# Kernel tuning notes

Hardware: AMD Instinct MI355X
Metric: run time of the kernel (lower is better)

Reference implementation:

```python
import jax, jax.numpy as jnp
import numpy as np

HEADS = 4
BN_EPS = 1e-5


def _linear_attention(x, heads):
    # x: [B, L, C]; per-head linear attention: softmax(Q,dim=feat) @ (softmax(K,dim=seq)^T @ V)
    B, L, C = x.shape
    dh = C // heads
    h = x.reshape(B, L, heads, dh)
    q = jax.nn.softmax(h, axis=-1)          # softmax over feature dim (dim=2 in torch)
    k = jax.nn.softmax(h, axis=1)           # softmax over sequence dim (dim=1 in torch)
    kv = jnp.einsum('blhd,blhe->bhde', k, h)   # [B, H, dh, dh]
    out = jnp.einsum('blhd,bhde->blhe', q, kv) # [B, L, H, dh]
    return out.reshape(B, L, C)


def setup_inputs() -> dict:
    key = jax.random.key(0)
    ks = jax.random.split(key, 10)
    B, C, L, DOUT, NB = 32, 32, 16384, 10, 3
    s = 0.1
    return {
        'x': jax.random.normal(ks[0], (B, C, L), jnp.float32),
        'fcW1': jax.random.normal(ks[1], (NB, C, C), jnp.float32) * s,
        'fcb1': jax.random.normal(ks[2], (NB, C), jnp.float32) * s,
        'fcW2': jax.random.normal(ks[3], (NB, C, C), jnp.float32) * s,
        'fcb2': jax.random.normal(ks[4], (NB, C), jnp.float32) * s,
        'Wh': jax.random.normal(ks[5], (C, C), jnp.float32) * s,
        'bh': jax.random.normal(ks[6], (C,), jnp.float32) * s,
        'bn_gamma': jnp.ones((C,), jnp.float32),
        'bn_beta': jnp.zeros((C,), jnp.float32),
        'bn_mean': jnp.zeros((C,), jnp.float32),
        'bn_var': jnp.ones((C,), jnp.float32),
        'Wf': jax.random.normal(ks[7], (C, DOUT), jnp.float32) * s,
        'bf': jax.random.normal(ks[8], (DOUT,), jnp.float32) * s,
    }


def reference(x, fcW1, fcb1, fcW2, fcb2, Wh, bh, bn_gamma, bn_beta, bn_mean, bn_var, Wf, bf):
    gelu = lambda t: jax.nn.gelu(t, approximate=False)  # torch default GELU is exact erf
    h = jnp.transpose(x, (0, 2, 1))  # [B, C, L] -> [B, L, C]
    n_blocks = fcW1.shape[0]
    for i in range(n_blocks):
        h = _linear_attention(h, HEADS)
        h = gelu(h @ fcW1[i] + fcb1[i])
        h = gelu(h @ fcW2[i] + fcb2[i])
    pooled = jnp.mean(h, axis=1)  # AdaptiveAvgPool1d(1) over L -> [B, C]
    y = pooled @ Wh + bh
    y = (y - bn_mean) * jax.lax.rsqrt(bn_var + BN_EPS) * bn_gamma + bn_beta  # BatchNorm1d (eval)
    y = gelu(y)
    return y @ Wf + bf
```

## Files before the change

### kernel.cpp

```cpp
#include <hip/hip_runtime.h>
#include <cstddef>

#define B_ 32
#define C_ 32
#define L_ 16384
#define H_ 4
#define DH_ 8
#define NB_ 3
#define DOUT_ 10
#define SEG_ 512
#define S_ (L_/SEG_)

#define WTILE 512
#define AST  40

typedef _Float16 f16_t;
typedef _Float16 f16x2 __attribute__((ext_vector_type(2)));
typedef _Float16 f16x8 __attribute__((ext_vector_type(8)));
typedef float    f32x4 __attribute__((ext_vector_type(4)));

__device__ __forceinline__ float gelu_f(float x){
    const float z  = fabsf(x) * 0.70710678118654752440f;
    const float t  = __builtin_amdgcn_rcpf(fmaf(0.3275911f, z, 1.0f));
    const float e  = __expf(-z * z);
    float p = fmaf(t, 1.061405429f, -1.453152027f);
    p = fmaf(t, p, 1.421413741f);
    p = fmaf(t, p, -0.284496736f);
    p = fmaf(t, p, 0.254829592f);
    const float erfz = 1.0f - p * t * e;
    const float phi  = fmaf(copysignf(erfz, x), 0.5f, 0.5f);
    return x * phi;
}

#define RED_MAX32(v) do{ v = fmaxf(v, __shfl_xor(v,1));  v = fmaxf(v, __shfl_xor(v,2)); \
                         v = fmaxf(v, __shfl_xor(v,4));  v = fmaxf(v, __shfl_xor(v,8)); \
                         v = fmaxf(v, __shfl_xor(v,16)); }while(0)
#define RED_SUM32(v) do{ v += __shfl_xor(v,1);  v += __shfl_xor(v,2); \
                         v += __shfl_xor(v,4);  v += __shfl_xor(v,8); \
                         v += __shfl_xor(v,16); }while(0)

__global__ __launch_bounds__(256) void stats_kernel(const float* __restrict__ h,
                                                    float* __restrict__ part){
    const int seg = blockIdx.x;
    const int hd  = blockIdx.y;
    const int b   = blockIdx.z;
    const int t   = threadIdx.x;
    const int d   = t >> 5;
    const int j   = t & 31;

    __shared__ float tile[8][SEG_];
    __shared__ float sm[8];

    const float* hb = h + (size_t)b * ((size_t)C_*L_) + (size_t)(hd*DH_)*L_ + (size_t)seg*SEG_;

    for (int f = t; f < 8*SEG_/4; f += 256){
        const int row = f >> 7;
        const int c4  = (f & 127) << 2;
        *(f32x4*)&tile[row][c4] = *(const f32x4*)&hb[(size_t)row*L_ + c4];
    }
    __syncthreads();

    float m = -INFINITY;
    #pragma unroll
    for (int i = 0; i < SEG_/32; i++) m = fmaxf(m, tile[d][j + 32*i]);
    RED_MAX32(m);
    if (j == 0) sm[d] = m;
    const float m_d = m;

    float s = 0.0f;
    float kv[8];
    #pragma unroll
    for (int e = 0; e < 8; e++) kv[e] = 0.0f;
    #pragma unroll
    for (int i = 0; i < SEG_/32; i++){
        const int k = j + 32*i;
        const float ek = __expf(tile[d][k] - m_d);
        s += ek;
        #pragma unroll
        for (int e = 0; e < 8; e++) kv[e] = fmaf(ek, tile[e][k], kv[e]);
    }
    RED_SUM32(s);
    #pragma unroll
    for (int e = 0; e < 8; e++){ RED_SUM32(kv[e]); }
    __syncthreads();

    float* po = part + (size_t)((b*H_ + hd)*S_ + seg) * 80;
    if (j == 0){
        po[8 + d] = s;
        #pragma unroll
        for (int e = 0; e < 8; e++) po[16 + d*8 + e] = kv[e];
    }
    if (t < 8) po[t] = sm[t];
}

template<bool LAST>
__global__ __launch_bounds__(256)
__attribute__((amdgpu_waves_per_eu(3, 4)))
void block_kernel(const float* hin,
                  float* hout,
                  const float* __restrict__ part,
                  const float* __restrict__ W1,
                  const float* __restrict__ b1,
                  const float* __restrict__ W2,
                  const float* __restrict__ b2,
                  float* pooled,
                  unsigned* done_ctr,
                  const float* __restrict__ Wh,
                  const float* __restrict__ bh,
                  const float* __restrict__ gam,
                  const float* __restrict__ bet,
                  const float* __restrict__ mean,
                  const float* __restrict__ var,
                  const float* __restrict__ Wf,
                  const float* __restrict__ bf,
                  float* __restrict__ out){
    __shared__ __align__(16) f16_t Ash[256*AST];
    __shared__ f16_t Bsh1[32*AST];
    __shared__ f16_t Bsh2[32*AST];
    __shared__ float sb1[32], sb2[32];
    __shared__ float kvsh[256];
    __shared__ float pool[32];
    __shared__ unsigned lastf;

    const int tid = threadIdx.x;
    const int b   = blockIdx.y;
    const int l0  = blockIdx.x * WTILE;
    const size_t base = (size_t)b * ((size_t)C_*L_);

    float h0[32], h1[32];
    #pragma unroll
    for (int c = 0; c < 32; c++) h0[c] = hin[base + (size_t)c*L_ + l0 + tid];
    #pragma unroll
    for (int c = 0; c < 32; c++) h1[c] = hin[base + (size_t)c*L_ + l0 + 256 + tid];

    for (int i = tid; i < 1024; i += 256){
        const int k = i >> 5, n = i & 31;
        Bsh1[n*AST + k] = (f16_t)W1[i];
        Bsh2[n*AST + k] = (f16_t)W2[i];
    }
    if (tid < 32){ sb1[tid] = b1[tid]; sb2[tid] = b2[tid]; }
    if (LAST && tid < 32) pool[tid] = 0.0f;

    {
        const int hh_t = tid >> 6;
        const int tt   = tid & 63;
        const int dd   = tt >> 3;
        const float* pp = part + (size_t)(b*H_ + hh_t) * S_ * 80;
        float M = -INFINITY;
        for (int s2 = 0; s2 < S_; s2++) M = fmaxf(M, pp[s2*80 + dd]);
        float ssum = 0.0f, kvs = 0.0f;
        for (int s2 = 0; s2 < S_; s2++){
            const float sc = __expf(pp[s2*80 + dd] - M);
            ssum = fmaf(pp[s2*80 + 8  + dd], sc, ssum);
            kvs  = fmaf(pp[s2*80 + 16 + tt], sc, kvs);
        }
        kvsh[tid] = kvs / ssum;
    }
    __syncthreads();

    const int wv   = tid >> 6;
    const int lane = tid & 63;
    const int lr   = lane & 15;
    const int lk   = lane >> 4;
    const f32x4 zero = {0.f, 0.f, 0.f, 0.f};

    auto attn_to_ash = [&](const float (&hh)[32], const bool preb){
        float attn[32];
        #pragma unroll
        for (int hd2 = 0; hd2 < 4; hd2++){
            float mq = hh[hd2*8];
            #pragma unroll
            for (int d2 = 1; d2 < 8; d2++) mq = fmaxf(mq, hh[hd2*8 + d2]);
            float es[8]; float qs = 0.f;
            #pragma unroll
            for (int d2 = 0; d2 < 8; d2++){ es[d2] = __expf(hh[hd2*8 + d2] - mq); qs += es[d2]; }
            const float inv = __builtin_amdgcn_rcpf(qs);
            #pragma unroll
            for (int e = 0; e < 8; e++){
                float acc = 0.f;
                #pragma unroll
                for (int d2 = 0; d2 < 8; d2++) acc += es[d2] * kvsh[hd2*64 + d2*8 + e];
                attn[hd2*8 + e] = acc * inv;
            }
        }
        if (preb) __syncthreads();
        #pragma unroll
        for (int k2 = 0; k2 < 32; k2 += 2){
            f16x2 pr = { (f16_t)attn[k2], (f16_t)attn[k2+1] };
            *(f16x2*)&Ash[tid*AST + k2] = pr;
        }
    };

    auto fc_and_out = [&](const int lofs){
        f16x8 a[4], bw[2];
        f32x4 d[8];
        #pragma unroll
        for (int mt = 0; mt < 4; mt++)
            a[mt] = *(const f16x8*)&Ash[(wv*64 + mt*16 + lr)*AST + lk*8];
        #pragma unroll
        for (int nt = 0; nt < 2; nt++)
            bw[nt] = *(const f16x8*)&Bsh1[(nt*16 + lr)*AST + lk*8];
        #pragma unroll
        for (int nt = 0; nt < 2; nt++)
            #pragma unroll
            for (int mt = 0; mt < 4; mt++)
                d[nt*4+mt] = __builtin_amdgcn_mfma_f32_16x16x32_f16(a[mt], bw[nt], zero, 0, 0, 0);

        #pragma unroll
        for (int nt = 0; nt < 2; nt++){
            const float bias = sb1[nt*16 + lr];
            #pragma unroll
            for (int mt = 0; mt < 4; mt++)
                #pragma unroll
                for (int r = 0; r < 4; r++){
                    const float v = gelu_f(d[nt*4+mt][r] + bias);
                    Ash[(wv*64 + mt*16 + lk*4 + r)*AST + (nt*16 + lr)] = (f16_t)v;
                }
        }

        #pragma unroll
        for (int mt = 0; mt < 4; mt++)
            a[mt] = *(const f16x8*)&Ash[(wv*64 + mt*16 + lr)*AST + lk*8];
        #pragma unroll
        for (int nt = 0; nt < 2; nt++)
            bw[nt] = *(const f16x8*)&Bsh2[(nt*16 + lr)*AST + lk*8];
        #pragma unroll
        for (int nt = 0; nt < 2; nt++)
            #pragma unroll
            for (int mt = 0; mt < 4; mt++)
                d[nt*4+mt] = __builtin_amdgcn_mfma_f32_16x16x32_f16(a[mt], bw[nt], zero, 0, 0, 0);

        #pragma unroll
        for (int nt = 0; nt < 2; nt++){
            const float bias = sb2[nt*16 + lr];
            #pragma unroll
            for (int mt = 0; mt < 4; mt++)
                #pragma unroll
                for (int r = 0; r < 4; r++)
                    d[nt*4+mt][r] = gelu_f(d[nt*4+mt][r] + bias);
        }

        if (!LAST){
            #pragma unroll
            for (int nt = 0; nt < 2; nt++)
                #pragma unroll
                for (int mt = 0; mt < 4; mt++)
                    *(f32x4*)&hout[base + (size_t)(nt*16 + lr)*L_
                                   + l0 + lofs + wv*64 + mt*16 + lk*4] = d[nt*4+mt];
        } else {
            #pragma unroll
            for (int nt = 0; nt < 2; nt++){
                float ps = 0.f;
                #pragma unroll
                for (int mt = 0; mt < 4; mt++)
                    ps += d[nt*4+mt][0] + d[nt*4+mt][1] + d[nt*4+mt][2] + d[nt*4+mt][3];
                atomicAdd(&pool[nt*16 + lr], ps);
            }
        }
    };

    attn_to_ash(h0, false);
    __syncthreads();
    fc_and_out(0);
    attn_to_ash(h1, true);
    __syncthreads();
    fc_and_out(256);

    if (LAST){
        __syncthreads();
        if (tid < 32){
            atomicAdd(&pooled[b*32 + tid], pool[tid]);
            __threadfence();
        }
        __syncthreads();
        if (tid == 0){
            const unsigned old = atomicAdd(done_ctr, 1u);
            lastf = (old == 1023u) ? 1u : 0u;
        }
        __syncthreads();
        if (lastf){
            __threadfence();
            float* y2 = (float*)Ash;
            const float invL = 1.0f / (float)L_;
            for (int i = tid; i < 1024; i += 256){
                const int bb = i >> 5, cc = i & 31;
                float acc = bh[cc];
                #pragma unroll
                for (int dd2 = 0; dd2 < 32; dd2++)
                    acc += (pooled[bb*32 + dd2] * invL) * Wh[dd2*32 + cc];
                acc = (acc - mean[cc]) * rsqrtf(var[cc] + 1e-5f) * gam[cc] + bet[cc];
                y2[i] = gelu_f(acc);
            }
            __syncthreads();
            for (int i = tid; i < B_*DOUT_; i += 256){
                const int b2 = i / DOUT_, j = i % DOUT_;
                float r = bf[j];
                #pragma unroll
                for (int c2 = 0; c2 < 32; c2++) r += y2[b2*32 + c2] * Wf[c2*DOUT_ + j];
                out[i] = r;
            }
        }
    }
}

extern "C" void kernel_launch(void* const* d_in, const int* in_sizes, int n_in,
                              void* d_out, int out_size, void* d_ws, size_t ws_size,
                              hipStream_t stream){
    (void)in_sizes; (void)n_in; (void)out_size; (void)ws_size;
    const float* x    = (const float*)d_in[0];
    const float* fW1  = (const float*)d_in[1];
    const float* fb1  = (const float*)d_in[2];
    const float* fW2  = (const float*)d_in[3];
    const float* fb2  = (const float*)d_in[4];
    const float* Wh   = (const float*)d_in[5];
    const float* bh   = (const float*)d_in[6];
    const float* gam  = (const float*)d_in[7];
    const float* bet  = (const float*)d_in[8];
    const float* mean = (const float*)d_in[9];
    const float* var  = (const float*)d_in[10];
    const float* Wf   = (const float*)d_in[11];
    const float* bf   = (const float*)d_in[12];
    float* out = (float*)d_out;

    float* hbuf    = (float*)d_ws;
    float* part    = hbuf + (size_t)B_*C_*L_;
    float* pooled  = part + (size_t)B_*H_*S_*80;
    unsigned* done = (unsigned*)(pooled + B_*C_);

    hipMemsetAsync(pooled, 0, (B_*C_ + 1)*sizeof(float), stream);

    dim3 sgrid(S_, H_, B_);
    dim3 bgrid(L_/WTILE, B_);

    stats_kernel<<<sgrid, 256, 0, stream>>>(x, part);
    block_kernel<false><<<bgrid, 256, 0, stream>>>(x, hbuf, part,
        fW1, fb1, fW2, fb2, nullptr, nullptr,
        nullptr, nullptr, nullptr, nullptr, nullptr, nullptr, nullptr, nullptr, nullptr);
    stats_kernel<<<sgrid, 256, 0, stream>>>(hbuf, part);
    block_kernel<false><<<bgrid, 256, 0, stream>>>(hbuf, hbuf, part,
        fW1 + C_*C_, fb1 + C_, fW2 + C_*C_, fb2 + C_, nullptr, nullptr,
        nullptr, nullptr, nullptr, nullptr, nullptr, nullptr, nullptr, nullptr, nullptr);
    stats_kernel<<<sgrid, 256, 0, stream>>>(hbuf, part);
    block_kernel<true><<<bgrid, 256, 0, stream>>>(hbuf, nullptr, part,
        fW1 + 2*C_*C_, fb1 + 2*C_, fW2 + 2*C_*C_, fb2 + 2*C_, pooled, done,
        Wh, bh, gam, bet, mean, var, Wf, bf, out);
}
```

Before: 303.1 us.

## Fuse all stats and block phases into one persistent cooperative kernel

Replaces six separate kernel launches and the memset with a single cooperative persistent kernel that loops over layers. Stats and MLP work items are distributed across a fixed grid sized from occupancy, with grid.sync between phases. The final head runs on workgroup 0 after the last grid barrier instead of through an atomic done-counter. This removes launch gaps and tail effects, at the cost of grid-wide barriers and fewer blocks in flight per phase.

```diff
diff --git a/kernel.cpp b/kernel.cpp
--- a/kernel.cpp
+++ b/kernel.cpp
@@ -1,18 +1,29 @@
 #include <hip/hip_runtime.h>
+#include <hip/hip_cooperative_groups.h>
 #include <cstddef>
+
+namespace cg = cooperative_groups;
 
 #define B_ 32
 #define C_ 32
 #define L_ 16384
 #define H_ 4
-#define DH_ 8
 #define NB_ 3
 #define DOUT_ 10
 #define SEG_ 512
 #define S_ (L_/SEG_)
-
-#define WTILE 512
-#define AST  40
+#define NSU (B_*H_*S_)
+#define NPAIR (B_*(L_/256)/2)
+#define AST 40
+
+#define OFF_SM    16384
+#define OFF_B1    20480
+#define OFF_B2    23040
+#define OFF_SB1   25600
+#define OFF_SB2   25728
+#define OFF_KV    25856
+#define OFF_POOL  26880
+#define LDS_BYTES 27008
 
 typedef _Float16 f16_t;
 typedef _Float16 f16x2 __attribute__((ext_vector_type(2)));
@@ -39,266 +50,255 @@
                          v += __shfl_xor(v,4);  v += __shfl_xor(v,8); \
                          v += __shfl_xor(v,16); }while(0)
 
-__global__ __launch_bounds__(256) void stats_kernel(const float* __restrict__ h,
-                                                    float* __restrict__ part){
-    const int seg = blockIdx.x;
-    const int hd  = blockIdx.y;
-    const int b   = blockIdx.z;
-    const int t   = threadIdx.x;
-    const int d   = t >> 5;
-    const int j   = t & 31;
-
-    __shared__ float tile[8][SEG_];
-    __shared__ float sm[8];
-
-    const float* hb = h + (size_t)b * ((size_t)C_*L_) + (size_t)(hd*DH_)*L_ + (size_t)seg*SEG_;
-
-    for (int f = t; f < 8*SEG_/4; f += 256){
-        const int row = f >> 7;
-        const int c4  = (f & 127) << 2;
-        *(f32x4*)&tile[row][c4] = *(const f32x4*)&hb[(size_t)row*L_ + c4];
-    }
-    __syncthreads();
-
-    float m = -INFINITY;
-    #pragma unroll
-    for (int i = 0; i < SEG_/32; i++) m = fmaxf(m, tile[d][j + 32*i]);
-    RED_MAX32(m);
-    if (j == 0) sm[d] = m;
-    const float m_d = m;
-
-    float s = 0.0f;
-    float kv[8];
-    #pragma unroll
-    for (int e = 0; e < 8; e++) kv[e] = 0.0f;
-    #pragma unroll
-    for (int i = 0; i < SEG_/32; i++){
-        const int k = j + 32*i;
-        const float ek = __expf(tile[d][k] - m_d);
-        s += ek;
+template<bool LASTL>
+__device__ __forceinline__
+void block_phase(char* LB, const float* __restrict__ src, float* __restrict__ hbuf,
+                 const float* __restrict__ part,
+                 const float* __restrict__ W1, const float* __restrict__ b1w,
+                 const float* __restrict__ W2, const float* __restrict__ b2w,
+                 float* __restrict__ pooled,
+                 const int tid, const int wg, const int nwg)
+{
+    f16_t* Ash   = (f16_t*)LB;
+    f16_t* Bs1   = (f16_t*)(LB + OFF_B1);
+    f16_t* Bs2   = (f16_t*)(LB + OFF_B2);
+    float* sb1   = (float*)(LB + OFF_SB1);
+    float* sb2   = (float*)(LB + OFF_SB2);
+    float* kvsh  = (float*)(LB + OFF_KV);
+    float* poolS = (float*)(LB + OFF_POOL);
+
+    for (int i = tid; i < 1024; i += 256){
+        const int k = i >> 5, n = i & 31;
+        Bs1[n*AST + k] = (f16_t)W1[i];
+        Bs2[n*AST + k] = (f16_t)W2[i];
+    }
+    if (tid < 32){ sb1[tid] = b1w[tid]; sb2[tid] = b2w[tid]; if (LASTL) poolS[tid] = 0.0f; }
+
+    const int wv = tid >> 6, lane = tid & 63, lr = lane & 15, lk = lane >> 4;
+    const f32x4 zero = {0.f, 0.f, 0.f, 0.f};
+
+    for (int pr = wg; pr < NPAIR; pr += nwg){
+        const int t0 = pr * 2;
+        const int b  = t0 >> 6;
+        const int l0 = (t0 & 63) << 8;
+        const size_t base = (size_t)b * ((size_t)C_*L_);
+
+        float h0[32], h1[32];
         #pragma unroll
-        for (int e = 0; e < 8; e++) kv[e] = fmaf(ek, tile[e][k], kv[e]);
-    }
-    RED_SUM32(s);
-    #pragma unroll
-    for (int e = 0; e < 8; e++){ RED_SUM32(kv[e]); }
-    __syncthreads();
-
-    float* po = part + (size_t)((b*H_ + hd)*S_ + seg) * 80;
-    if (j == 0){
-        po[8 + d] = s;
+        for (int c = 0; c < 32; c++) h0[c] = src[base + (size_t)c*L_ + l0 + tid];
         #pragma unroll
-        for (int e = 0; e < 8; e++) po[16 + d*8 + e] = kv[e];
-    }
-    if (t < 8) po[t] = sm[t];
+        for (int c = 0; c < 32; c++) h1[c] = src[base + (size_t)c*L_ + l0 + 256 + tid];
+
+        __syncthreads();
+
+        {
+            const int hh = tid >> 6, tt = tid & 63, dd = tt >> 3;
+            const float* pp = part + (size_t)(b*H_ + hh) * S_ * 80;
+            float M = -INFINITY;
+            for (int s2 = 0; s2 < S_; s2++) M = fmaxf(M, pp[s2*80 + dd]);
+            float ssum = 0.0f, kvs = 0.0f;
+            for (int s2 = 0; s2 < S_; s2++){
+                const float sc = __expf(pp[s2*80 + dd] - M);
+                ssum = fmaf(pp[s2*80 + 8  + dd], sc, ssum);
+                kvs  = fmaf(pp[s2*80 + 16 + tt], sc, kvs);
+            }
+            kvsh[tid] = kvs / ssum;
+        }
+        __syncthreads();
+
+        auto do_tile = [&](const float (&hv)[32], const int lofs){
+            float attn[32];
+            #pragma unroll
+            for (int hd2 = 0; hd2 < 4; hd2++){
+                float mq = hv[hd2*8];
+                #pragma unroll
+                for (int d2 = 1; d2 < 8; d2++) mq = fmaxf(mq, hv[hd2*8 + d2]);
+                float es[8]; float qs = 0.f;
+                #pragma unroll
+                for (int d2 = 0; d2 < 8; d2++){ es[d2] = __expf(hv[hd2*8 + d2] - mq); qs += es[d2]; }
+                const float inv = __builtin_amdgcn_rcpf(qs);
+                #pragma unroll
+                for (int e = 0; e < 8; e++){
+                    float acc = 0.f;
+                    #pragma unroll
+                    for (int d2 = 0; d2 < 8; d2++) acc += es[d2] * kvsh[hd2*64 + d2*8 + e];
+                    attn[hd2*8 + e] = acc * inv;
+                }
+            }
+            #pragma unroll
+            for (int k2 = 0; k2 < 32; k2 += 2){
+                f16x2 pv = { (f16_t)attn[k2], (f16_t)attn[k2+1] };
+                *(f16x2*)&Ash[tid*AST + k2] = pv;
+            }
+            f16x8 a[4], bw[2];
+            f32x4 d[8];
+            #pragma unroll
+            for (int mt = 0; mt < 4; mt++)
+                a[mt] = *(const f16x8*)&Ash[(wv*64 + mt*16 + lr)*AST + lk*8];
+            #pragma unroll
+            for (int nt = 0; nt < 2; nt++)
+                bw[nt] = *(const f16x8*)&Bs1[(nt*16 + lr)*AST + lk*8];
+            #pragma unroll
+            for (int nt = 0; nt < 2; nt++)
+                #pragma unroll
+                for (int mt = 0; mt < 4; mt++)
+                    d[nt*4+mt] = __builtin_amdgcn_mfma_f32_16x16x32_f16(a[mt], bw[nt], zero, 0, 0, 0);
+            #pragma unroll
+            for (int nt = 0; nt < 2; nt++){
+                const float bias = sb1[nt*16 + lr];
+                #pragma unroll
+                for (int mt = 0; mt < 4; mt++)
+                    #pragma unroll
+                    for (int r = 0; r < 4; r++){
+                        const float v = gelu_f(d[nt*4+mt][r] + bias);
+                        Ash[(wv*64 + mt*16 + lk*4 + r)*AST + (nt*16 + lr)] = (f16_t)v;
+                    }
+            }
+            #pragma unroll
+            for (int mt = 0; mt < 4; mt++)
+                a[mt] = *(const f16x8*)&Ash[(wv*64 + mt*16 + lr)*AST + lk*8];
+            #pragma unroll
+            for (int nt = 0; nt < 2; nt++)
+                bw[nt] = *(const f16x8*)&Bs2[(nt*16 + lr)*AST + lk*8];
+            #pragma unroll
+            for (int nt = 0; nt < 2; nt++)
+                #pragma unroll
+                for (int mt = 0; mt < 4; mt++)
+                    d[nt*4+mt] = __builtin_amdgcn_mfma_f32_16x16x32_f16(a[mt], bw[nt], zero, 0, 0, 0);
+            #pragma unroll
+            for (int nt = 0; nt < 2; nt++){
+                const float bias = sb2[nt*16 + lr];
+                #pragma unroll
+                for (int mt = 0; mt < 4; mt++)
+                    #pragma unroll
+                    for (int r = 0; r < 4; r++)
+                        d[nt*4+mt][r] = gelu_f(d[nt*4+mt][r] + bias);
+            }
+            if (!LASTL){
+                #pragma unroll
+                for (int nt = 0; nt < 2; nt++)
+                    #pragma unroll
+                    for (int mt = 0; mt < 4; mt++)
+                        *(f32x4*)&hbuf[base + (size_t)(nt*16 + lr)*L_
+                                       + lofs + wv*64 + mt*16 + lk*4] = d[nt*4+mt];
+            } else {
+                #pragma unroll
+                for (int nt = 0; nt < 2; nt++){
+                    float ps = 0.f;
+                    #pragma unroll
+                    for (int mt = 0; mt < 4; mt++)
+                        ps += d[nt*4+mt][0] + d[nt*4+mt][1] + d[nt*4+mt][2] + d[nt*4+mt][3];
+                    atomicAdd(&poolS[nt*16 + lr], ps);
+                }
+            }
+        };
+
+        do_tile(h0, l0);
+        do_tile(h1, l0 + 256);
+
+        if (LASTL){
+            __syncthreads();
+            if (tid < 32){ atomicAdd(&pooled[b*32 + tid], poolS[tid]); poolS[tid] = 0.0f; }
+        }
+    }
 }
 
-template<bool LAST>
 __global__ __launch_bounds__(256)
 __attribute__((amdgpu_waves_per_eu(3, 4)))
-void block_kernel(const float* hin,
-                  float* hout,
-                  const float* __restrict__ part,
-                  const float* __restrict__ W1,
-                  const float* __restrict__ b1,
-                  const float* __restrict__ W2,
-                  const float* __restrict__ b2,
-                  float* pooled,
-                  unsigned* done_ctr,
-                  const float* __restrict__ Wh,
-                  const float* __restrict__ bh,
-                  const float* __restrict__ gam,
-                  const float* __restrict__ bet,
-                  const float* __restrict__ mean,
-                  const float* __restrict__ var,
-                  const float* __restrict__ Wf,
-                  const float* __restrict__ bf,
-                  float* __restrict__ out){
-    __shared__ __align__(16) f16_t Ash[256*AST];
-    __shared__ f16_t Bsh1[32*AST];
-    __shared__ f16_t Bsh2[32*AST];
-    __shared__ float sb1[32], sb2[32];
-    __shared__ float kvsh[256];
-    __shared__ float pool[32];
-    __shared__ unsigned lastf;
-
+void fused_all(const float* __restrict__ x, float* __restrict__ hbuf,
+               float* __restrict__ part, float* __restrict__ pooled,
+               const float* __restrict__ fW1, const float* __restrict__ fb1,
+               const float* __restrict__ fW2, const float* __restrict__ fb2,
+               const float* __restrict__ Wh,  const float* __restrict__ bh,
+               const float* __restrict__ gam, const float* __restrict__ bet,
+               const float* __restrict__ mean,const float* __restrict__ var,
+               const float* __restrict__ Wf,  const float* __restrict__ bf,
+               float* __restrict__ out)
+{
+    __shared__ __align__(16) char LB[LDS_BYTES];
     const int tid = threadIdx.x;
-    const int b   = blockIdx.y;
-    const int l0  = blockIdx.x * WTILE;
-    const size_t base = (size_t)b * ((size_t)C_*L_);
-
-    float h0[32], h1[32];
-    #pragma unroll
-    for (int c = 0; c < 32; c++) h0[c] = hin[base + (size_t)c*L_ + l0 + tid];
-    #pragma unroll
-    for (int c = 0; c < 32; c++) h1[c] = hin[base + (size_t)c*L_ + l0 + 256 + tid];
-
-    for (int i = tid; i < 1024; i += 256){
-        const int k = i >> 5, n = i & 31;
-        Bsh1[n*AST + k] = (f16_t)W1[i];
-        Bsh2[n*AST + k] = (f16_t)W2[i];
-    }
-    if (tid < 32){ sb1[tid] = b1[tid]; sb2[tid] = b2[tid]; }
-    if (LAST && tid < 32) pool[tid] = 0.0f;
-
-    {
-        const int hh_t = tid >> 6;
-        const int tt   = tid & 63;
-        const int dd   = tt >> 3;
-        const float* pp = part + (size_t)(b*H_ + hh_t) * S_ * 80;
-        float M = -INFINITY;
-        for (int s2 = 0; s2 < S_; s2++) M = fmaxf(M, pp[s2*80 + dd]);
-        float ssum = 0.0f, kvs = 0.0f;
-        for (int s2 = 0; s2 < S_; s2++){
-            const float sc = __expf(pp[s2*80 + dd] - M);
-            ssum = fmaf(pp[s2*80 + 8  + dd], sc, ssum);
-            kvs  = fmaf(pp[s2*80 + 16 + tt], sc, kvs);
-        }
-        kvsh[tid] = kvs / ssum;
-    }
-    __syncthreads();
-
-    const int wv   = tid >> 6;
-    const int lane = tid & 63;
-    const int lr   = lane & 15;
-    const int lk   = lane >> 4;
-    const f32x4 zero = {0.f, 0.f, 0.f, 0.f};
-
-    auto attn_to_ash = [&](const float (&hh)[32], const bool preb){
-        float attn[32];
-        #pragma unroll
-        for (int hd2 = 0; hd2 < 4; hd2++){
-            float mq = hh[hd2*8];
-            #pragma unroll
-            for (int d2 = 1; d2 < 8; d2++) mq = fmaxf(mq, hh[hd2*8 + d2]);
-            float es[8]; float qs = 0.f;
-            #pragma unroll
-            for (int d2 = 0; d2 < 8; d2++){ es[d2] = __expf(hh[hd2*8 + d2] - mq); qs += es[d2]; }
-            const float inv = __builtin_amdgcn_rcpf(qs);
-            #pragma unroll
-            for (int e = 0; e < 8; e++){
-                float acc = 0.f;
-                #pragma unroll
-                for (int d2 = 0; d2 < 8; d2++) acc += es[d2] * kvsh[hd2*64 + d2*8 + e];
-                attn[hd2*8 + e] = acc * inv;
-            }
-        }
-        if (preb) __syncthreads();
-        #pragma unroll
-        for (int k2 = 0; k2 < 32; k2 += 2){
-            f16x2 pr = { (f16_t)attn[k2], (f16_t)attn[k2+1] };
-            *(f16x2*)&Ash[tid*AST + k2] = pr;
-        }
-    };
-
-    auto fc_and_out = [&](const int lofs){
-        f16x8 a[4], bw[2];
-        f32x4 d[8];
-        #pragma unroll
-        for (int mt = 0; mt < 4; mt++)
-            a[mt] = *(const f16x8*)&Ash[(wv*64 + mt*16 + lr)*AST + lk*8];
-        #pragma unroll
-        for (int nt = 0; nt < 2; nt++)
-            bw[nt] = *(const f16x8*)&Bsh1[(nt*16 + lr)*AST + lk*8];
-        #pragma unroll
-        for (int nt = 0; nt < 2; nt++)
-            #pragma unroll
-            for (int mt = 0; mt < 4; mt++)
-                d[nt*4+mt] = __builtin_amdgcn_mfma_f32_16x16x32_f16(a[mt], bw[nt], zero, 0, 0, 0);
-
-        #pragma unroll
-        for (int nt = 0; nt < 2; nt++){
-            const float bias = sb1[nt*16 + lr];
-            #pragma unroll
-            for (int mt = 0; mt < 4; mt++)
-                #pragma unroll
-                for (int r = 0; r < 4; r++){
-                    const float v = gelu_f(d[nt*4+mt][r] + bias);
-                    Ash[(wv*64 + mt*16 + lk*4 + r)*AST + (nt*16 + lr)] = (f16_t)v;
-                }
-        }
-
-        #pragma unroll
-        for (int mt = 0; mt < 4; mt++)
-            a[mt] = *(const f16x8*)&Ash[(wv*64 + mt*16 + lr)*AST + lk*8];
-        #pragma unroll
-        for (int nt = 0; nt < 2; nt++)
-            bw[nt] = *(const f16x8*)&Bsh2[(nt*16 + lr)*AST + lk*8];
-        #pragma unroll
-        for (int nt = 0; nt < 2; nt++)
-            #pragma unroll
-            for (int mt = 0; mt < 4; mt++)
-                d[nt*4+mt] = __builtin_amdgcn_mfma_f32_16x16x32_f16(a[mt], bw[nt], zero, 0, 0, 0);
-
-        #pragma unroll
-        for (int nt = 0; nt < 2; nt++){
-            const float bias = sb2[nt*16 + lr];
-            #pragma unroll
-            for (int mt = 0; mt < 4; mt++)
-                #pragma unroll
-                for (int r = 0; r < 4; r++)
-                    d[nt*4+mt][r] = gelu_f(d[nt*4+mt][r] + bias);
-        }
-
-        if (!LAST){
-            #pragma unroll
-            for (int nt = 0; nt < 2; nt++)
-                #pragma unroll
-                for (int mt = 0; mt < 4; mt++)
-                    *(f32x4*)&hout[base + (size_t)(nt*16 + lr)*L_
-                                   + l0 + lofs + wv*64 + mt*16 + lk*4] = d[nt*4+mt];
-        } else {
-            #pragma unroll
-            for (int nt = 0; nt < 2; nt++){
-                float ps = 0.f;
-                #pragma unroll
-                for (int mt = 0; mt < 4; mt++)
-                    ps += d[nt*4+mt][0] + d[nt*4+mt][1] + d[nt*4+mt][2] + d[nt*4+mt][3];
-                atomicAdd(&pool[nt*16 + lr], ps);
-            }
-        }
-    };
-
-    attn_to_ash(h0, false);
-    __syncthreads();
-    fc_and_out(0);
-    attn_to_ash(h1, true);
-    __syncthreads();
-    fc_and_out(256);
-
-    if (LAST){
+    const int wg  = blockIdx.x;
+    const int nwg = gridDim.x;
+    cg::grid_group grid = cg::this_grid();
+
+    if (wg == 0) for (int i = tid; i < B_*C_; i += 256) pooled[i] = 0.0f;
+
+    #pragma unroll 1
+    for (int layer = 0; layer < NB_; ++layer){
+        const float* src = layer ? hbuf : x;
+
+        {
+            float* tile = (float*)LB;
+            float* sm   = (float*)(LB + OFF_SM);
+            const int dd = tid >> 5, j = tid & 31;
+            for (int u = wg; u < NSU; u += nwg){
+                const int seg = u & 31, hd = (u >> 5) & 3, b = u >> 7;
+                const float* hb = src + (size_t)b*((size_t)C_*L_)
+                                      + (size_t)(hd*8)*L_ + (size_t)seg*SEG_;
+                for (int f = tid; f < 8*SEG_/4; f += 256){
+                    const int row = f >> 7, c4 = (f & 127) << 2;
+                    *(f32x4*)&tile[row*SEG_ + c4] = *(const f32x4*)&hb[(size_t)row*L_ + c4];
+                }
+                __syncthreads();
+                float m = -INFINITY;
+                #pragma unroll
+                for (int i = 0; i < SEG_/32; i++) m = fmaxf(m, tile[dd*SEG_ + j + 32*i]);
+                RED_MAX32(m);
+                if (j == 0) sm[dd] = m;
+                float s = 0.0f, kv[8];
+                #pragma unroll
+                for (int e = 0; e < 8; e++) kv[e] = 0.0f;
+                #pragma unroll
+                for (int i = 0; i < SEG_/32; i++){
+                    const int k = j + 32*i;
+                    const float ek = __expf(tile[dd*SEG_ + k] - m);
+                    s += ek;
+                    #pragma unroll
+                    for (int e = 0; e < 8; e++) kv[e] = fmaf(ek, tile[e*SEG_ + k], kv[e]);
+                }
+                RED_SUM32(s);
+                #pragma unroll
+                for (int e = 0; e < 8; e++){ RED_SUM32(kv[e]); }
+                __syncthreads();
+                float* po = part + (size_t)u * 80;
+                if (j == 0){
+                    po[8 + dd] = s;
+                    #pragma unroll
+                    for (int e = 0; e < 8; e++) po[16 + dd*8 + e] = kv[e];
+                }
+                if (tid < 8) po[tid] = sm[tid];
+            }
+        }
+        grid.sync();
+
+        if (layer < NB_-1)
+            block_phase<false>(LB, src, hbuf, part, fW1 + layer*C_*C_, fb1 + layer*C_,
+                               fW2 + layer*C_*C_, fb2 + layer*C_, pooled, tid, wg, nwg);
+        else
+            block_phase<true >(LB, src, hbuf, part, fW1 + layer*C_*C_, fb1 + layer*C_,
+                               fW2 + layer*C_*C_, fb2 + layer*C_, pooled, tid, wg, nwg);
+        grid.sync();
+    }
+
+    if (wg == 0){
+        float* y2 = (float*)LB;
+        const float invL = 1.0f / (float)L_;
+        for (int i = tid; i < B_*C_; i += 256){
+            const int bb = i >> 5, cc = i & 31;
+            float acc = bh[cc];
+            #pragma unroll
+            for (int d2 = 0; d2 < 32; d2++)
+                acc += (pooled[bb*32 + d2] * invL) * Wh[d2*32 + cc];
+            acc = (acc - mean[cc]) * rsqrtf(var[cc] + 1e-5f) * gam[cc] + bet[cc];
+            y2[i] = gelu_f(acc);
+        }
         __syncthreads();
-        if (tid < 32){
-            atomicAdd(&pooled[b*32 + tid], pool[tid]);
-            __threadfence();
-        }
-        __syncthreads();
-        if (tid == 0){
-            const unsigned old = atomicAdd(done_ctr, 1u);
-            lastf = (old == 1023u) ? 1u : 0u;
-        }
-        __syncthreads();
-        if (lastf){
-            __threadfence();
-            float* y2 = (float*)Ash;
-            const float invL = 1.0f / (float)L_;
-            for (int i = tid; i < 1024; i += 256){
-                const int bb = i >> 5, cc = i & 31;
-                float acc = bh[cc];
-                #pragma unroll
-                for (int dd2 = 0; dd2 < 32; dd2++)
-                    acc += (pooled[bb*32 + dd2] * invL) * Wh[dd2*32 + cc];
-                acc = (acc - mean[cc]) * rsqrtf(var[cc] + 1e-5f) * gam[cc] + bet[cc];
-                y2[i] = gelu_f(acc);
-            }
-            __syncthreads();
-            for (int i = tid; i < B_*DOUT_; i += 256){
-                const int b2 = i / DOUT_, j = i % DOUT_;
-                float r = bf[j];
-                #pragma unroll
-                for (int c2 = 0; c2 < 32; c2++) r += y2[b2*32 + c2] * Wf[c2*DOUT_ + j];
-                out[i] = r;
-            }
+        for (int i = tid; i < B_*DOUT_; i += 256){
+            const int b2 = i / DOUT_, jj = i % DOUT_;
+            float r = bf[jj];
+            #pragma unroll
+            for (int c2 = 0; c2 < 32; c2++) r += y2[b2*32 + c2] * Wf[c2*DOUT_ + jj];
+            out[i] = r;
         }
     }
 }
@@ -322,26 +322,34 @@
     const float* bf   = (const float*)d_in[12];
     float* out = (float*)d_out;
 
-    float* hbuf    = (float*)d_ws;
-    float* part    = hbuf + (size_t)B_*C_*L_;
-    float* pooled  = part + (size_t)B_*H_*S_*80;
-    unsigned* done = (unsigned*)(pooled + B_*C_);
-
-    hipMemsetAsync(pooled, 0, (B_*C_ + 1)*sizeof(float), stream);
-
-    dim3 sgrid(S_, H_, B_);
-    dim3 bgrid(L_/WTILE, B_);
-
-    stats_kernel<<<sgrid, 256, 0, stream>>>(x, part);
-    block_kernel<false><<<bgrid, 256, 0, stream>>>(x, hbuf, part,
-        fW1, fb1, fW2, fb2, nullptr, nullptr,
-        nullptr, nullptr, nullptr, nullptr, nullptr, nullptr, nullptr, nullptr, nullptr);
-    stats_kernel<<<sgrid, 256, 0, stream>>>(hbuf, part);
-    block_kernel<false><<<bgrid, 256, 0, stream>>>(hbuf, hbuf, part,
-        fW1 + C_*C_, fb1 + C_, fW2 + C_*C_, fb2 + C_, nullptr, nullptr,
-        nullptr, nullptr, nullptr, nullptr, nullptr, nullptr, nullptr, nullptr, nullptr);
-    stats_kernel<<<sgrid, 256, 0, stream>>>(hbuf, part);
-    block_kernel<true><<<bgrid, 256, 0, stream>>>(hbuf, nullptr, part,
-        fW1 + 2*C_*C_, fb1 + 2*C_, fW2 + 2*C_*C_, fb2 + 2*C_, pooled, done,
-        Wh, bh, gam, bet, mean, var, Wf, bf, out);
+    float* hbuf   = (float*)d_ws;
+    float* part   = hbuf + (size_t)B_*C_*L_;
+    float* pooled = part + (size_t)NSU*80;
+
+    static int g_grid = 0;
+    if (g_grid == 0){
+        int nb = 0;
+        if (hipOccupancyMaxActiveBlocksPerMultiprocessor(
+                &nb, reinterpret_cast<const void*>(&fused_all), 256, 0) != hipSuccess
+            || nb <= 0) nb = 3;
+        int ncu = 256;
+        int dev = 0;
+        if (hipGetDevice(&dev) == hipSuccess){
+            hipDeviceProp_t prop;
+            if (hipGetDeviceProperties(&prop, dev) == hipSuccess && prop.multiProcessorCount > 0)
+                ncu = prop.multiProcessorCount;
+        }
+        long g = (long)nb * ncu;
+        if (g > 1024) g = 1024;
+        if (g < 128)  g = 128;
+        g_grid = (int)g;
+    }
+
+    void* args[] = { (void*)&x, (void*)&hbuf, (void*)&part, (void*)&pooled,
+                     (void*)&fW1, (void*)&fb1, (void*)&fW2, (void*)&fb2,
+                     (void*)&Wh, (void*)&bh, (void*)&gam, (void*)&bet,
+                     (void*)&mean, (void*)&var, (void*)&Wf, (void*)&bf,
+                     (void*)&out };
+    hipLaunchCooperativeKernel(reinterpret_cast<const void*>(&fused_all),
+                               dim3(g_grid), dim3(256), args, 0, stream);
 }
```

Result: slower. 709.4 us (+134.0%).
